# Optimization experiments

Measured on AMD Instinct MI355X. Metric: run time of the kernel, lower is better.

Reference implementation:

```python
import jax, jax.numpy as jnp
import numpy as np

N, D, NUM_CLASSES = 4096, 1024, 64


def setup_inputs() -> dict:
    key = jax.random.key(0)
    k1, k2 = jax.random.split(key)
    inputs = jax.random.normal(k1, (N, D), dtype=jnp.float32)
    labels = jax.random.randint(k2, (N,), 0, NUM_CLASSES, dtype=jnp.int64)
    return {"inputs": inputs, "labels": labels}


def reference(inputs, labels):
    # dist_mat = inputs @ inputs.T  (raw dot-product 'cosine_dist', no normalization)
    dist = jnp.matmul(inputs, inputs.T)  # [N, N]
    n = inputs.shape[0]
    same = labels[:, None] == labels[None, :]          # [N, N]
    eye = jnp.eye(n, dtype=bool)
    is_pos = same & ~eye                               # same label, excluding self
    is_neg = ~same                                     # different label
    # hardest-positive: +2 penalty on non-positive entries, then row argmin
    d_ap = jnp.where(is_pos, dist, dist + 2.0)
    # 'easiest' negative: +2 penalty on non-negative entries, then row argmin
    d_an = jnp.where(is_neg, dist, dist + 2.0)
    id_ap = jnp.argmin(d_ap, axis=1)                   # [N]
    id_an = jnp.argmin(d_an, axis=1)                   # [N]
    # (The original also computes a semi-hard id_an_semi, but returns id_an;
    #  that block is dead code w.r.t. the output, so it is omitted.)
    return (inputs[id_ap], inputs[id_an])
```

## Files before the change

### kernel.cpp

```cpp
#include <hip/hip_runtime.h>
#include <cstdint>

#define N 4096
#define D 1024
#define KC_COUNT (D / 32)
#define TB (N / 128)
#define NBLK (TB * (TB + 1) / 2)

typedef _Float16 f16;
typedef __attribute__((ext_vector_type(4))) _Float16 f16x4;
typedef __attribute__((ext_vector_type(8))) _Float16 f16x8;
typedef __attribute__((ext_vector_type(4))) float f32x4;

__device__ __forceinline__ unsigned int orderable(float f) {
    unsigned int b = __float_as_uint(f);
    return (b & 0x80000000u) ? ~b : (b | 0x80000000u);
}

__device__ __forceinline__ void async_copy16(const f16* g, f16* l) {
    __builtin_amdgcn_global_load_lds(
        (const __attribute__((address_space(1))) uint32_t*)(const void*)g,
        (__attribute__((address_space(3))) uint32_t*)(void*)l,
        16 , 0 , 0 );
}

#define ROW_PAD 8
#define ROW_STRIDE (D + ROW_PAD)
__global__ __launch_bounds__(256) void split_swizzle(
    const float* __restrict__ X, f16* __restrict__ Xsw,
    unsigned long long* __restrict__ keys)
{
    __shared__ f16 Hs[16 * ROW_STRIDE];
    __shared__ f16 Ls[16 * ROW_STRIDE];
    const int tid = threadIdx.x;
    const int rg = blockIdx.x;
    if (tid < 32) keys[rg * 32 + tid] = 0xFFFFFFFFFFFFFFFFull;

    const float4* src = (const float4*)(X + (size_t)rg * 16 * D);
#pragma unroll
    for (int it = 0; it < 16; ++it) {
        const int idx4 = it * 256 + tid;
        const int row = idx4 >> 8;
        const int k4 = (idx4 & 255) * 4;
        const float4 v = src[idx4];
        const float xs[4] = {v.x, v.y, v.z, v.w};
        f16x4 h, l;
#pragma unroll
        for (int i = 0; i < 4; ++i) {
            f16 hh = (f16)xs[i];
            h[i] = hh;
            l[i] = (f16)(xs[i] - (float)hh);
        }
        *(f16x4*)(Hs + row * ROW_STRIDE + k4) = h;
        *(f16x4*)(Ls + row * ROW_STRIDE + k4) = l;
    }
    __syncthreads();
#pragma unroll
    for (int hl = 0; hl < 2; ++hl) {
        const f16* lds = hl ? Ls : Hs;
#pragma unroll
        for (int it = 0; it < 8; ++it) {
            const int o = it * 256 + tid;
            const int kc = o >> 6, lo_ = o & 63;
            const int q = lo_ >> 4, m = lo_ & 15;
            const uint4 v = *(const uint4*)(lds + m * ROW_STRIDE + kc * 32 + q * 8);
            *(uint4*)(Xsw + (((size_t)rg * KC_COUNT + kc) * 2 + hl) * 512 + lo_ * 8) = v;
        }
    }
}

__global__ __launch_bounds__(256) void gemm_argmin_sym(
    const f16* __restrict__ Xsw, const int* __restrict__ labels,
    unsigned long long* __restrict__ keys_ap,
    unsigned long long* __restrict__ keys_an)
{
    __shared__ f16 As[8 * 2 * 512];
    __shared__ f16 Bs[8 * 2 * 512];
    __shared__ int labM[128], labN[128];

    int r = blockIdx.x, bi = 0;
    while (r >= TB - bi) { r -= TB - bi; ++bi; }
    const int bj = bi + r;

    const int tid = threadIdx.x;
    const int lane = tid & 63;
    const int w = tid >> 6;
    const int wr = w >> 1, wc = w & 1;
    const int rowBase = bi * 128, colBase = bj * 128;

    if (tid < 128) labM[tid] = labels[rowBase + tid];
    else           labN[tid - 128] = labels[colBase + tid - 128];

    f32x4 acc[4][4];
#pragma unroll
    for (int mi = 0; mi < 4; ++mi)
#pragma unroll
        for (int ni = 0; ni < 4; ++ni) acc[mi][ni] = (f32x4){0.f, 0.f, 0.f, 0.f};

    const f16* g[8];
    f16* lp[8];
#pragma unroll
    for (int j = 0; j < 8; ++j) {
        int L = w * 8 + j;
        int isB = L >> 4, rem = L & 15, rgL = rem >> 1, hl = rem & 1;
        int rgG = (isB ? bj : bi) * 8 + rgL;
        g[j] = Xsw + ((((size_t)rgG * KC_COUNT) * 2 + hl) * 64 + lane) * 8;
        lp[j] = (isB ? Bs : As) + (rgL * 2 + hl) * 512;
    }

    for (int kc = 0; kc < KC_COUNT; ++kc) {
#pragma unroll
        for (int j = 0; j < 8; ++j)
            async_copy16(g[j] + (size_t)kc * 1024, lp[j]);
        __syncthreads();

        f16x8 ah[4], al[4], bh[4], bl[4];
#pragma unroll
        for (int t2 = 0; t2 < 4; ++t2) {
            int rgA = wr * 4 + t2, rgB = wc * 4 + t2;
            ah[t2] = *(const f16x8*)(As + (rgA * 2 + 0) * 512 + lane * 8);
            al[t2] = *(const f16x8*)(As + (rgA * 2 + 1) * 512 + lane * 8);
            bh[t2] = *(const f16x8*)(Bs + (rgB * 2 + 0) * 512 + lane * 8);
            bl[t2] = *(const f16x8*)(Bs + (rgB * 2 + 1) * 512 + lane * 8);
        }
#pragma unroll
        for (int mi = 0; mi < 4; ++mi)
#pragma unroll
            for (int ni = 0; ni < 4; ++ni) {
                acc[mi][ni] = __builtin_amdgcn_mfma_f32_16x16x32_f16(
                    ah[mi], bh[ni], acc[mi][ni], 0, 0, 0);
                acc[mi][ni] = __builtin_amdgcn_mfma_f32_16x16x32_f16(
                    ah[mi], bl[ni], acc[mi][ni], 0, 0, 0);
                acc[mi][ni] = __builtin_amdgcn_mfma_f32_16x16x32_f16(
                    al[mi], bh[ni], acc[mi][ni], 0, 0, 0);
            }
        __syncthreads();
    }

    const int g16 = lane >> 4, c16 = lane & 15;

#pragma unroll
    for (int mi = 0; mi < 4; ++mi) {
#pragma unroll
        for (int reg = 0; reg < 4; ++reg) {
            const int rloc = wr * 64 + mi * 16 + g16 * 4 + reg;
            const int i = rowBase + rloc;
            const int li = labM[rloc];
            float bestAp = __builtin_huge_valf(); int jAp = 0;
            float bestAn = __builtin_huge_valf(); int jAn = 0;
#pragma unroll
            for (int ni = 0; ni < 4; ++ni) {
                const int cloc = wc * 64 + ni * 16 + c16;
                const int jcol = colBase + cloc;
                const int lj = labN[cloc];
                const float v = acc[mi][ni][reg];
                const bool same = (li == lj);
                const float vap = (same && (i != jcol)) ? v : v + 2.0f;
                const float van = (!same) ? v : v + 2.0f;
                if (vap < bestAp) { bestAp = vap; jAp = jcol; }
                if (van < bestAn) { bestAn = van; jAn = jcol; }
            }
            unsigned long long kap =
                ((unsigned long long)orderable(bestAp) << 32) | (unsigned)jAp;
            unsigned long long kan =
                ((unsigned long long)orderable(bestAn) << 32) | (unsigned)jAn;
#pragma unroll
            for (int off = 1; off < 16; off <<= 1) {
                unsigned long long o = __shfl_xor(kap, off); kap = o < kap ? o : kap;
                o = __shfl_xor(kan, off); kan = o < kan ? o : kan;
            }
            if (c16 == 0) {
                atomicMin(&keys_ap[i], kap);
                atomicMin(&keys_an[i], kan);
            }
        }
    }

    if (bi != bj) {
#pragma unroll
        for (int ni = 0; ni < 4; ++ni) {
            const int cloc = wc * 64 + ni * 16 + c16;
            const int j = colBase + cloc;
            const int lj = labN[cloc];
            float bestAp = __builtin_huge_valf(); int iAp = 0;
            float bestAn = __builtin_huge_valf(); int iAn = 0;
#pragma unroll
            for (int mi = 0; mi < 4; ++mi)
#pragma unroll
                for (int reg = 0; reg < 4; ++reg) {
                    const int rloc = wr * 64 + mi * 16 + g16 * 4 + reg;
                    const int i = rowBase + rloc;
                    const int li = labM[rloc];
                    const float v = acc[mi][ni][reg];
                    const bool same = (li == lj);
                    const float vap = same ? v : v + 2.0f;
                    const float van = (!same) ? v : v + 2.0f;
                    if (vap < bestAp) { bestAp = vap; iAp = i; }
                    if (van < bestAn) { bestAn = van; iAn = i; }
                }
            unsigned long long kap =
                ((unsigned long long)orderable(bestAp) << 32) | (unsigned)iAp;
            unsigned long long kan =
                ((unsigned long long)orderable(bestAn) << 32) | (unsigned)iAn;
#pragma unroll
            for (int off = 16; off < 64; off <<= 1) {
                unsigned long long o = __shfl_xor(kap, off); kap = o < kap ? o : kap;
                o = __shfl_xor(kan, off); kan = o < kan ? o : kan;
            }
            if (g16 == 0) {
                atomicMin(&keys_ap[j], kap);
                atomicMin(&keys_an[j], kan);
            }
        }
    }
}

__global__ void gather_rows(const float* __restrict__ A,
                            const unsigned long long* __restrict__ keys_ap,
                            const unsigned long long* __restrict__ keys_an,
                            float* __restrict__ out)
{
    const int row = blockIdx.x;
    const int t = threadIdx.x;
    const int ja = (int)(keys_ap[row] & 0xFFFFFFFFull);
    const int jn = (int)(keys_an[row] & 0xFFFFFFFFull);
    const float4* Av = (const float4*)A;
    float4* Ov = (float4*)out;
    Ov[(size_t)row * (D / 4) + t]       = Av[(size_t)ja * (D / 4) + t];
    Ov[(size_t)(N + row) * (D / 4) + t] = Av[(size_t)jn * (D / 4) + t];
}

extern "C" void kernel_launch(void* const* d_in, const int* in_sizes, int n_in,
                              void* d_out, int out_size, void* d_ws, size_t ws_size,
                              hipStream_t stream) {
    const float* A = (const float*)d_in[0];
    const int* labels = (const int*)d_in[1];
    float* out = (float*)d_out;

    unsigned long long* keys = (unsigned long long*)d_ws;
    f16* Xsw = (f16*)((char*)d_ws + 65536);

    split_swizzle<<<N / 16, 256, 0, stream>>>(A, Xsw, keys);
    gemm_argmin_sym<<<NBLK, 256, 0, stream>>>(Xsw, labels, keys, keys + N);
    gather_rows<<<N, 256, 0, stream>>>(A, keys, keys + N, out);
}
```

Before: 176.0 us.

## Double-buffer LDS tiles to prefetch next K-chunk during MFMA compute

Splits the A/B shared-memory tiles into two buffers and issues the async global-to-LDS copies for chunk kc+1 before computing on chunk kc. This takes the copy latency off the per-iteration critical path, and the leading barrier goes away. Labels are now read straight from global memory into registers in the epilogue instead of being staged in LDS. The trade-off is twice the LDS per block, which can lower occupancy, and more register pressure from the label arrays.

```diff
diff --git a/kernel.cpp b/kernel.cpp
--- a/kernel.cpp
+++ b/kernel.cpp
@@ -74,9 +74,8 @@
     unsigned long long* __restrict__ keys_ap,
     unsigned long long* __restrict__ keys_an)
 {
-    __shared__ f16 As[8 * 2 * 512];
-    __shared__ f16 Bs[8 * 2 * 512];
-    __shared__ int labM[128], labN[128];
+    __shared__ f16 As[2][8 * 2 * 512];
+    __shared__ f16 Bs[2][8 * 2 * 512];
 
     int r = blockIdx.x, bi = 0;
     while (r >= TB - bi) { r -= TB - bi; ++bi; }
@@ -88,9 +87,6 @@
     const int wr = w >> 1, wc = w & 1;
     const int rowBase = bi * 128, colBase = bj * 128;
 
-    if (tid < 128) labM[tid] = labels[rowBase + tid];
-    else           labN[tid - 128] = labels[colBase + tid - 128];
-
     f32x4 acc[4][4];
 #pragma unroll
     for (int mi = 0; mi < 4; ++mi)
@@ -98,30 +94,40 @@
         for (int ni = 0; ni < 4; ++ni) acc[mi][ni] = (f32x4){0.f, 0.f, 0.f, 0.f};
 
     const f16* g[8];
-    f16* lp[8];
+    f16* lp0[8];
+    f16* lp1[8];
 #pragma unroll
     for (int j = 0; j < 8; ++j) {
         int L = w * 8 + j;
         int isB = L >> 4, rem = L & 15, rgL = rem >> 1, hl = rem & 1;
         int rgG = (isB ? bj : bi) * 8 + rgL;
         g[j] = Xsw + ((((size_t)rgG * KC_COUNT) * 2 + hl) * 64 + lane) * 8;
-        lp[j] = (isB ? Bs : As) + (rgL * 2 + hl) * 512;
-    }
+        lp0[j] = (isB ? Bs[0] : As[0]) + (rgL * 2 + hl) * 512;
+        lp1[j] = (isB ? Bs[1] : As[1]) + (rgL * 2 + hl) * 512;
+    }
+
+#pragma unroll
+    for (int j = 0; j < 8; ++j) async_copy16(g[j], lp0[j]);
+    __syncthreads();
 
     for (int kc = 0; kc < KC_COUNT; ++kc) {
-#pragma unroll
-        for (int j = 0; j < 8; ++j)
-            async_copy16(g[j] + (size_t)kc * 1024, lp[j]);
-        __syncthreads();
-
+        const int cur = kc & 1;
+        if (kc + 1 < KC_COUNT) {
+#pragma unroll
+            for (int j = 0; j < 8; ++j)
+                async_copy16(g[j] + (size_t)(kc + 1) * 1024, cur ? lp0[j] : lp1[j]);
+        }
+
+        const f16* A_ = As[cur];
+        const f16* B_ = Bs[cur];
         f16x8 ah[4], al[4], bh[4], bl[4];
 #pragma unroll
         for (int t2 = 0; t2 < 4; ++t2) {
             int rgA = wr * 4 + t2, rgB = wc * 4 + t2;
-            ah[t2] = *(const f16x8*)(As + (rgA * 2 + 0) * 512 + lane * 8);
-            al[t2] = *(const f16x8*)(As + (rgA * 2 + 1) * 512 + lane * 8);
-            bh[t2] = *(const f16x8*)(Bs + (rgB * 2 + 0) * 512 + lane * 8);
-            bl[t2] = *(const f16x8*)(Bs + (rgB * 2 + 1) * 512 + lane * 8);
+            ah[t2] = *(const f16x8*)(A_ + (rgA * 2 + 0) * 512 + lane * 8);
+            al[t2] = *(const f16x8*)(A_ + (rgA * 2 + 1) * 512 + lane * 8);
+            bh[t2] = *(const f16x8*)(B_ + (rgB * 2 + 0) * 512 + lane * 8);
+            bl[t2] = *(const f16x8*)(B_ + (rgB * 2 + 1) * 512 + lane * 8);
         }
 #pragma unroll
         for (int mi = 0; mi < 4; ++mi)
@@ -139,22 +145,29 @@
 
     const int g16 = lane >> 4, c16 = lane & 15;
 
+    int ljv[4], liv[4][4];
+#pragma unroll
+    for (int ni = 0; ni < 4; ++ni) ljv[ni] = labels[colBase + wc * 64 + ni * 16 + c16];
+#pragma unroll
+    for (int mi = 0; mi < 4; ++mi)
+#pragma unroll
+        for (int reg = 0; reg < 4; ++reg)
+            liv[mi][reg] = labels[rowBase + wr * 64 + mi * 16 + g16 * 4 + reg];
+
 #pragma unroll
     for (int mi = 0; mi < 4; ++mi) {
 #pragma unroll
         for (int reg = 0; reg < 4; ++reg) {
             const int rloc = wr * 64 + mi * 16 + g16 * 4 + reg;
             const int i = rowBase + rloc;
-            const int li = labM[rloc];
+            const int li = liv[mi][reg];
             float bestAp = __builtin_huge_valf(); int jAp = 0;
             float bestAn = __builtin_huge_valf(); int jAn = 0;
 #pragma unroll
             for (int ni = 0; ni < 4; ++ni) {
-                const int cloc = wc * 64 + ni * 16 + c16;
-                const int jcol = colBase + cloc;
-                const int lj = labN[cloc];
+                const int jcol = colBase + wc * 64 + ni * 16 + c16;
                 const float v = acc[mi][ni][reg];
-                const bool same = (li == lj);
+                const bool same = (li == ljv[ni]);
                 const float vap = (same && (i != jcol)) ? v : v + 2.0f;
                 const float van = (!same) ? v : v + 2.0f;
                 if (vap < bestAp) { bestAp = vap; jAp = jcol; }
@@ -179,20 +192,17 @@
     if (bi != bj) {
 #pragma unroll
         for (int ni = 0; ni < 4; ++ni) {
-            const int cloc = wc * 64 + ni * 16 + c16;
-            const int j = colBase + cloc;
-            const int lj = labN[cloc];
+            const int j = colBase + wc * 64 + ni * 16 + c16;
+            const int lj = ljv[ni];
             float bestAp = __builtin_huge_valf(); int iAp = 0;
             float bestAn = __builtin_huge_valf(); int iAn = 0;
 #pragma unroll
             for (int mi = 0; mi < 4; ++mi)
 #pragma unroll
                 for (int reg = 0; reg < 4; ++reg) {
-                    const int rloc = wr * 64 + mi * 16 + g16 * 4 + reg;
-                    const int i = rowBase + rloc;
-                    const int li = labM[rloc];
+                    const int i = rowBase + wr * 64 + mi * 16 + g16 * 4 + reg;
                     const float v = acc[mi][ni][reg];
-                    const bool same = (li == lj);
+                    const bool same = (liv[mi][reg] == lj);
                     const float vap = same ? v : v + 2.0f;
                     const float van = (!same) ? v : v + 2.0f;
                     if (vap < bestAp) { bestAp = vap; iAp = i; }
```

New measurement: 198.7 us. +12.9%, slower.

## Shrink GEMM tiles to 96 with padded N and split swizzle over K

Applied to the files above, without the earlier changes.

Changes the symmetric GEMM tile from 128 to 96 rows, padding the row count to a multiple of 96 with zero rows, which raises the block count and sets a launch-bounds occupancy hint. Labels are loaded directly into registers instead of LDS, and the split/swizzle kernel now uses four blocks per row group with smaller shared buffers and zero-fills the padding. The aim is better CU load balance and occupancy, at the cost of less data reuse per tile and extra padded work.

```diff
diff --git a/kernel.cpp b/kernel.cpp
--- a/kernel.cpp
+++ b/kernel.cpp
@@ -4,8 +4,10 @@
 #define N 4096
 #define D 1024
 #define KC_COUNT (D / 32)
-#define TB (N / 128)
-#define NBLK (TB * (TB + 1) / 2)
+#define NP 4128
+#define RGP (NP / 16)
+#define TG (NP / 96)
+#define NBLK (TG * (TG + 1) / 2)
 
 typedef _Float16 f16;
 typedef __attribute__((ext_vector_type(4))) _Float16 f16x4;
@@ -24,109 +26,118 @@
         16 , 0 , 0 );
 }
 
-#define ROW_PAD 8
-#define ROW_STRIDE (D + ROW_PAD)
+#define KSPAN 256
+#define SS_STRIDE (KSPAN + 24)
 __global__ __launch_bounds__(256) void split_swizzle(
     const float* __restrict__ X, f16* __restrict__ Xsw,
     unsigned long long* __restrict__ keys)
 {
-    __shared__ f16 Hs[16 * ROW_STRIDE];
-    __shared__ f16 Ls[16 * ROW_STRIDE];
+    __shared__ f16 Hs[16 * SS_STRIDE];
+    __shared__ f16 Ls[16 * SS_STRIDE];
     const int tid = threadIdx.x;
-    const int rg = blockIdx.x;
-    if (tid < 32) keys[rg * 32 + tid] = 0xFFFFFFFFFFFFFFFFull;
-
-    const float4* src = (const float4*)(X + (size_t)rg * 16 * D);
-#pragma unroll
-    for (int it = 0; it < 16; ++it) {
-        const int idx4 = it * 256 + tid;
-        const int row = idx4 >> 8;
-        const int k4 = (idx4 & 255) * 4;
-        const float4 v = src[idx4];
+    const int bid = blockIdx.x;
+    const int rg = bid >> 2, kq = bid & 3;
+    if (bid < 32) keys[bid * 256 + tid] = 0xFFFFFFFFFFFFFFFFull;
+
+    if (rg >= 256) {
+        const uint4 z = {0, 0, 0, 0};
+#pragma unroll
+        for (int i = 0; i < 4; ++i) {
+            const int o = i * 256 + tid;
+            const int kcl = o >> 7, rem = o & 127;
+            const int kc = kq * 8 + kcl;
+            *(uint4*)(Xsw + (((size_t)rg * KC_COUNT + kc) * 2) * 512 + rem * 8) = z;
+        }
+        return;
+    }
+
+#pragma unroll
+    for (int i = 0; i < 4; ++i) {
+        const int idx4 = i * 256 + tid;
+        const int row = idx4 >> 6, c4 = idx4 & 63;
+        const float4 v = *(const float4*)(X + (size_t)(rg * 16 + row) * D + kq * KSPAN + c4 * 4);
         const float xs[4] = {v.x, v.y, v.z, v.w};
         f16x4 h, l;
 #pragma unroll
-        for (int i = 0; i < 4; ++i) {
-            f16 hh = (f16)xs[i];
-            h[i] = hh;
-            l[i] = (f16)(xs[i] - (float)hh);
-        }
-        *(f16x4*)(Hs + row * ROW_STRIDE + k4) = h;
-        *(f16x4*)(Ls + row * ROW_STRIDE + k4) = l;
+        for (int e = 0; e < 4; ++e) {
+            f16 hh = (f16)xs[e];
+            h[e] = hh;
+            l[e] = (f16)(xs[e] - (float)hh);
+        }
+        *(f16x4*)(Hs + row * SS_STRIDE + c4 * 4) = h;
+        *(f16x4*)(Ls + row * SS_STRIDE + c4 * 4) = l;
     }
     __syncthreads();
+
 #pragma unroll
     for (int hl = 0; hl < 2; ++hl) {
         const f16* lds = hl ? Ls : Hs;
 #pragma unroll
-        for (int it = 0; it < 8; ++it) {
-            const int o = it * 256 + tid;
-            const int kc = o >> 6, lo_ = o & 63;
+        for (int i = 0; i < 2; ++i) {
+            const int o = i * 256 + tid;
+            const int kcl = o >> 6, lo_ = o & 63;
             const int q = lo_ >> 4, m = lo_ & 15;
-            const uint4 v = *(const uint4*)(lds + m * ROW_STRIDE + kc * 32 + q * 8);
+            const uint4 v = *(const uint4*)(lds + m * SS_STRIDE + kcl * 32 + q * 8);
+            const int kc = kq * 8 + kcl;
             *(uint4*)(Xsw + (((size_t)rg * KC_COUNT + kc) * 2 + hl) * 512 + lo_ * 8) = v;
         }
     }
 }
 
-__global__ __launch_bounds__(256) void gemm_argmin_sym(
+__global__ __launch_bounds__(256, 4) void gemm_argmin_sym(
     const f16* __restrict__ Xsw, const int* __restrict__ labels,
     unsigned long long* __restrict__ keys_ap,
     unsigned long long* __restrict__ keys_an)
 {
-    __shared__ f16 As[8 * 2 * 512];
-    __shared__ f16 Bs[8 * 2 * 512];
-    __shared__ int labM[128], labN[128];
-
-    int r = blockIdx.x, bi = 0;
-    while (r >= TB - bi) { r -= TB - bi; ++bi; }
-    const int bj = bi + r;
+    __shared__ f16 As[6 * 2 * 512];
+    __shared__ f16 Bs[6 * 2 * 512];
+
+    int r = blockIdx.x, ti = 0;
+    while (r >= TG - ti) { r -= TG - ti; ++ti; }
+    const int tj = ti + r;
 
     const int tid = threadIdx.x;
     const int lane = tid & 63;
     const int w = tid >> 6;
     const int wr = w >> 1, wc = w & 1;
-    const int rowBase = bi * 128, colBase = bj * 128;
-
-    if (tid < 128) labM[tid] = labels[rowBase + tid];
-    else           labN[tid - 128] = labels[colBase + tid - 128];
-
-    f32x4 acc[4][4];
-#pragma unroll
-    for (int mi = 0; mi < 4; ++mi)
-#pragma unroll
-        for (int ni = 0; ni < 4; ++ni) acc[mi][ni] = (f32x4){0.f, 0.f, 0.f, 0.f};
-
-    const f16* g[8];
-    f16* lp[8];
-#pragma unroll
-    for (int j = 0; j < 8; ++j) {
-        int L = w * 8 + j;
-        int isB = L >> 4, rem = L & 15, rgL = rem >> 1, hl = rem & 1;
-        int rgG = (isB ? bj : bi) * 8 + rgL;
+    const int rowBase = ti * 96, colBase = tj * 96;
+
+    f32x4 acc[3][3];
+#pragma unroll
+    for (int mi = 0; mi < 3; ++mi)
+#pragma unroll
+        for (int ni = 0; ni < 3; ++ni) acc[mi][ni] = (f32x4){0.f, 0.f, 0.f, 0.f};
+
+    const f16* g[6];
+    f16* lp[6];
+#pragma unroll
+    for (int j = 0; j < 6; ++j) {
+        int c = w * 6 + j;
+        int isB = c >= 12, rem = isB ? c - 12 : c, rgL = rem >> 1, hl = rem & 1;
+        int rgG = (isB ? tj : ti) * 6 + rgL;
         g[j] = Xsw + ((((size_t)rgG * KC_COUNT) * 2 + hl) * 64 + lane) * 8;
         lp[j] = (isB ? Bs : As) + (rgL * 2 + hl) * 512;
     }
 
     for (int kc = 0; kc < KC_COUNT; ++kc) {
 #pragma unroll
-        for (int j = 0; j < 8; ++j)
+        for (int j = 0; j < 6; ++j)
             async_copy16(g[j] + (size_t)kc * 1024, lp[j]);
         __syncthreads();
 
-        f16x8 ah[4], al[4], bh[4], bl[4];
-#pragma unroll
-        for (int t2 = 0; t2 < 4; ++t2) {
-            int rgA = wr * 4 + t2, rgB = wc * 4 + t2;
+        f16x8 ah[3], al[3], bh[3], bl[3];
+#pragma unroll
+        for (int t2 = 0; t2 < 3; ++t2) {
+            int rgA = wr * 3 + t2, rgB = wc * 3 + t2;
             ah[t2] = *(const f16x8*)(As + (rgA * 2 + 0) * 512 + lane * 8);
             al[t2] = *(const f16x8*)(As + (rgA * 2 + 1) * 512 + lane * 8);
             bh[t2] = *(const f16x8*)(Bs + (rgB * 2 + 0) * 512 + lane * 8);
             bl[t2] = *(const f16x8*)(Bs + (rgB * 2 + 1) * 512 + lane * 8);
         }
 #pragma unroll
-        for (int mi = 0; mi < 4; ++mi)
-#pragma unroll
-            for (int ni = 0; ni < 4; ++ni) {
+        for (int mi = 0; mi < 3; ++mi)
+#pragma unroll
+            for (int ni = 0; ni < 3; ++ni) {
                 acc[mi][ni] = __builtin_amdgcn_mfma_f32_16x16x32_f16(
                     ah[mi], bh[ni], acc[mi][ni], 0, 0, 0);
                 acc[mi][ni] = __builtin_amdgcn_mfma_f32_16x16x32_f16(
@@ -139,22 +150,33 @@
 
     const int g16 = lane >> 4, c16 = lane & 15;
 
-#pragma unroll
-    for (int mi = 0; mi < 4; ++mi) {
+    int ljv[3], liv[3][4];
+#pragma unroll
+    for (int ni = 0; ni < 3; ++ni) {
+        const int j = colBase + wc * 48 + ni * 16 + c16;
+        ljv[ni] = (j < N) ? labels[j] : -1;
+    }
+#pragma unroll
+    for (int mi = 0; mi < 3; ++mi)
 #pragma unroll
         for (int reg = 0; reg < 4; ++reg) {
-            const int rloc = wr * 64 + mi * 16 + g16 * 4 + reg;
-            const int i = rowBase + rloc;
-            const int li = labM[rloc];
+            const int i = rowBase + wr * 48 + mi * 16 + g16 * 4 + reg;
+            liv[mi][reg] = (i < N) ? labels[i] : -1;
+        }
+
+#pragma unroll
+    for (int mi = 0; mi < 3; ++mi) {
+#pragma unroll
+        for (int reg = 0; reg < 4; ++reg) {
+            const int i = rowBase + wr * 48 + mi * 16 + g16 * 4 + reg;
+            const int li = liv[mi][reg];
             float bestAp = __builtin_huge_valf(); int jAp = 0;
             float bestAn = __builtin_huge_valf(); int jAn = 0;
 #pragma unroll
-            for (int ni = 0; ni < 4; ++ni) {
-                const int cloc = wc * 64 + ni * 16 + c16;
-                const int jcol = colBase + cloc;
-                const int lj = labN[cloc];
+            for (int ni = 0; ni < 3; ++ni) {
+                const int jcol = colBase + wc * 48 + ni * 16 + c16;
                 const float v = acc[mi][ni][reg];
-                const bool same = (li == lj);
+                const bool same = (li == ljv[ni]);
                 const float vap = (same && (i != jcol)) ? v : v + 2.0f;
                 const float van = (!same) ? v : v + 2.0f;
                 if (vap < bestAp) { bestAp = vap; jAp = jcol; }
@@ -169,30 +191,27 @@
                 unsigned long long o = __shfl_xor(kap, off); kap = o < kap ? o : kap;
                 o = __shfl_xor(kan, off); kan = o < kan ? o : kan;
             }
-            if (c16 == 0) {
+            if (c16 == 0 && i < N) {
                 atomicMin(&keys_ap[i], kap);
                 atomicMin(&keys_an[i], kan);
             }
         }
     }
 
-    if (bi != bj) {
-#pragma unroll
-        for (int ni = 0; ni < 4; ++ni) {
-            const int cloc = wc * 64 + ni * 16 + c16;
-            const int j = colBase + cloc;
-            const int lj = labN[cloc];
+    if (ti != tj) {
+#pragma unroll
+        for (int ni = 0; ni < 3; ++ni) {
+            const int j = colBase + wc * 48 + ni * 16 + c16;
+            const int lj = ljv[ni];
             float bestAp = __builtin_huge_valf(); int iAp = 0;
             float bestAn = __builtin_huge_valf(); int iAn = 0;
 #pragma unroll
-            for (int mi = 0; mi < 4; ++mi)
+            for (int mi = 0; mi < 3; ++mi)
 #pragma unroll
                 for (int reg = 0; reg < 4; ++reg) {
-                    const int rloc = wr * 64 + mi * 16 + g16 * 4 + reg;
-                    const int i = rowBase + rloc;
-                    const int li = labM[rloc];
+                    const int i = rowBase + wr * 48 + mi * 16 + g16 * 4 + reg;
                     const float v = acc[mi][ni][reg];
-                    const bool same = (li == lj);
+                    const bool same = (liv[mi][reg] == lj);
                     const float vap = same ? v : v + 2.0f;
                     const float van = (!same) ? v : v + 2.0f;
                     if (vap < bestAp) { bestAp = vap; iAp = i; }
@@ -207,7 +226,7 @@
                 unsigned long long o = __shfl_xor(kap, off); kap = o < kap ? o : kap;
                 o = __shfl_xor(kan, off); kan = o < kan ? o : kan;
             }
-            if (g16 == 0) {
+            if (g16 == 0 && j < N) {
                 atomicMin(&keys_ap[j], kap);
                 atomicMin(&keys_an[j], kan);
             }
@@ -240,7 +259,7 @@
     unsigned long long* keys = (unsigned long long*)d_ws;
     f16* Xsw = (f16*)((char*)d_ws + 65536);
 
-    split_swizzle<<<N / 16, 256, 0, stream>>>(A, Xsw, keys);
+    split_swizzle<<<RGP * 4, 256, 0, stream>>>(A, Xsw, keys);
     gemm_argmin_sym<<<NBLK, 256, 0, stream>>>(Xsw, labels, keys, keys + N);
     gather_rows<<<N, 256, 0, stream>>>(A, keys, keys + N, out);
 }
```

Result: faster. 155.2 us (-11.8%).
